# Kernel optimization log

Hardware: AMD Instinct MI355X
Metric: run time of the kernel (lower is better)

The kernel has to match this reference:

```python
import jax, jax.numpy as jnp
import numpy as np

B, S, H, NH = 2, 2048, 1024, 16
HD = H // NH

def setup_inputs() -> dict:
    key = jax.random.key(0)
    ks = jax.random.split(key, 10)
    f = lambda k, shape, scale: jax.random.normal(k, shape, dtype=jnp.float32) * scale
    return {
        "hidden_states": f(ks[0], (B, S, H), 1.0),
        "attention_mask": f(ks[1], (B, 1, S, S), 1.0),
        # static weights: randn * static_ratio(0.9); dynamic: randn * 0.01
        "q_static": f(ks[2], (H, H), 0.9), "q_dynamic": f(ks[3], (H, H), 0.01),
        "k_static": f(ks[4], (H, H), 0.9), "k_dynamic": f(ks[5], (H, H), 0.01),
        "v_static": f(ks[6], (H, H), 0.9), "v_dynamic": f(ks[7], (H, H), 0.01),
        "o_static": f(ks[8], (H, H), 0.9), "o_dynamic": f(ks[9], (H, H), 0.01),
    }

def _split_heads(x):
    # [B, S, H] -> [B, NH, S, HD]
    b, s, _ = x.shape
    return x.reshape(b, s, NH, HD).transpose(0, 2, 1, 3)

def reference(hidden_states, attention_mask,
              q_static, q_dynamic, k_static, k_dynamic,
              v_static, v_dynamic, o_static, o_dynamic):
    # DualWeightLinear: y = x @ (static + dynamic)^T  (no bias)
    q = hidden_states @ (q_static + q_dynamic).T
    k = hidden_states @ (k_static + k_dynamic).T
    v = hidden_states @ (v_static + v_dynamic).T
    q, k, v = _split_heads(q), _split_heads(k), _split_heads(v)  # [B,NH,S,HD]
    scale = 1.0 / np.sqrt(HD).astype(np.float32)
    scores = jnp.einsum('bhqd,bhkd->bhqk', q, k) * scale  # [B,NH,S,S]
    scores = scores + attention_mask  # additive mask, broadcast over heads
    attn = jax.nn.softmax(scores, axis=-1)
    out = jnp.einsum('bhqk,bhkd->bhqd', attn, v)
    out = out.transpose(0, 2, 1, 3).reshape(hidden_states.shape[0], hidden_states.shape[1], H)
    return out @ (o_static + o_dynamic).T
```

## Files before the change

### kernel.cpp

```cpp
#include <hip/hip_runtime.h>
#include <hip/hip_bf16.h>
#include <stdint.h>

#define BB 2
#define SS 2048
#define HH 1024
#define NHH 16
#define HDD 64
#define MM (BB*SS)
#define N4SEG (HH*HH/4)

typedef __attribute__((ext_vector_type(8))) short short8;
typedef __attribute__((ext_vector_type(4))) float f32x4;
typedef __attribute__((ext_vector_type(4))) unsigned short u16x4;
typedef __attribute__((ext_vector_type(4))) unsigned int u32x4;

__device__ __forceinline__ unsigned short f2bf(float x){
  unsigned u = __float_as_uint(x);
  u += 0x7fffu + ((u >> 16) & 1u);
  return (unsigned short)(u >> 16);
}
__device__ __forceinline__ float bf2f(unsigned short h){
  return __uint_as_float(((unsigned)h) << 16);
}
__device__ __forceinline__ unsigned short f2bf_fast(float x){
  __hip_bfloat16 hb = __float2bfloat16(x);
  return *reinterpret_cast<unsigned short*>(&hb);
}

__global__ void k_split(const float* __restrict__ in, unsigned short* __restrict__ hi,
                        unsigned short* __restrict__ lo, int n4){
  int i = blockIdx.x * blockDim.x + threadIdx.x;
  if (i >= n4) return;
  f32x4 x = ((const f32x4*)in)[i];
  u16x4 h, l;
  #pragma unroll
  for (int j = 0; j < 4; ++j){
    unsigned short hb = f2bf(x[j]);
    h[j] = hb;
    l[j] = f2bf(x[j] - bf2f(hb));
  }
  ((u16x4*)hi)[i] = h;
  ((u16x4*)lo)[i] = l;
}

__global__ void k_wprep(const float* __restrict__ qs, const float* __restrict__ qd,
                        const float* __restrict__ ks, const float* __restrict__ kd,
                        const float* __restrict__ vs, const float* __restrict__ vd,
                        const float* __restrict__ os_, const float* __restrict__ od,
                        unsigned short* __restrict__ wqh, unsigned short* __restrict__ wql,
                        unsigned short* __restrict__ wkh, unsigned short* __restrict__ wkl,
                        unsigned short* __restrict__ wv,  unsigned short* __restrict__ wo){
  int i = blockIdx.x * blockDim.x + threadIdx.x;
  int seg = i >> 18;
  int j = i & (N4SEG - 1);
  const float *pa, *pb; unsigned short *ph, *pl = nullptr;
  if      (seg == 0){ pa = qs; pb = qd; ph = wqh; pl = wql; }
  else if (seg == 1){ pa = ks; pb = kd; ph = wkh; pl = wkl; }
  else if (seg == 2){ pa = vs; pb = vd; ph = wv; }
  else              { pa = os_; pb = od; ph = wo; }
  f32x4 x = ((const f32x4*)pa)[j] + ((const f32x4*)pb)[j];
  u16x4 h, l;
  #pragma unroll
  for (int c = 0; c < 4; ++c){
    unsigned short hb = f2bf(x[c]);
    h[c] = hb;
    l[c] = f2bf(x[c] - bf2f(hb));
  }
  ((u16x4*)ph)[j] = h;
  if (pl) ((u16x4*)pl)[j] = l;
}

__global__ __launch_bounds__(256, 2)
void proj_fused(const unsigned short* __restrict__ hsh, const unsigned short* __restrict__ hsl,
                const unsigned short* __restrict__ wqh, const unsigned short* __restrict__ wql,
                const unsigned short* __restrict__ wkh, const unsigned short* __restrict__ wkl,
                const unsigned short* __restrict__ wv,
                unsigned short* __restrict__ qhB, unsigned short* __restrict__ qlB,
                unsigned short* __restrict__ khB, unsigned short* __restrict__ klB,
                unsigned short* __restrict__ vtB)
{
  __shared__ unsigned short Ash[128*32], Asl[128*32], Bsh[128*32], Bsl[128*32];
  const int tid = threadIdx.x;
  const int nb0 = blockIdx.x * 128;
  const int mb0 = blockIdx.y * 128;
  const int kind = nb0 >> 10;
  const int ncol0 = nb0 & 1023;
  const int w  = tid >> 6, lane = tid & 63;
  const int wr = w >> 1,  wc = w & 1;
  const int lg = lane >> 4, lr = lane & 15;

  const unsigned short* Bh = (kind == 0 ? wqh : (kind == 1 ? wkh : wv)) + (size_t)ncol0 * HH;
  const unsigned short* Bl = (kind == 0 ? wql : wkl) + (size_t)ncol0 * HH;
  const unsigned short* Ahb = hsh + (size_t)mb0 * HH;
  const unsigned short* Alb = hsl + (size_t)mb0 * HH;

  f32x4 zero4 = {0.f, 0.f, 0.f, 0.f};
  f32x4 acc[4][4];
  #pragma unroll
  for (int mi = 0; mi < 4; ++mi)
    #pragma unroll
    for (int ni = 0; ni < 4; ++ni) acc[mi][ni] = zero4;

  for (int kb = 0; kb < HH; kb += 32) {
    __syncthreads();
    #pragma unroll
    for (int i = 0; i < 2; ++i){
      int c = i*256 + tid;
      int row = c >> 2, off = (c & 3) << 3;
      size_t go = (size_t)row * HH + kb + off;
      __builtin_amdgcn_global_load_lds(
          (const __attribute__((address_space(1))) void*)(Ahb + go),
          (__attribute__((address_space(3))) void*)(&Ash[c*8]), 16, 0, 0);
      __builtin_amdgcn_global_load_lds(
          (const __attribute__((address_space(1))) void*)(Alb + go),
          (__attribute__((address_space(3))) void*)(&Asl[c*8]), 16, 0, 0);
      __builtin_amdgcn_global_load_lds(
          (const __attribute__((address_space(1))) void*)(Bh + go),
          (__attribute__((address_space(3))) void*)(&Bsh[c*8]), 16, 0, 0);
      if (kind < 2)
        __builtin_amdgcn_global_load_lds(
            (const __attribute__((address_space(1))) void*)(Bl + go),
            (__attribute__((address_space(3))) void*)(&Bsl[c*8]), 16, 0, 0);
    }
    __syncthreads();
    short8 ah4[4], al4[4], bh4[4], bl4[4];
    #pragma unroll
    for (int mi = 0; mi < 4; ++mi){
      int ro = (wr*64 + mi*16 + lr)*32 + lg*8;
      ah4[mi] = *(const short8*)&Ash[ro];
      al4[mi] = *(const short8*)&Asl[ro];
    }
    #pragma unroll
    for (int ni = 0; ni < 4; ++ni){
      int ro = (wc*64 + ni*16 + lr)*32 + lg*8;
      bh4[ni] = *(const short8*)&Bsh[ro];
    }
    if (kind < 2) {
      #pragma unroll
      for (int ni = 0; ni < 4; ++ni){
        int ro = (wc*64 + ni*16 + lr)*32 + lg*8;
        bl4[ni] = *(const short8*)&Bsl[ro];
      }
      #pragma unroll
      for (int mi = 0; mi < 4; ++mi)
        #pragma unroll
        for (int ni = 0; ni < 4; ++ni){
          acc[mi][ni] = __builtin_amdgcn_mfma_f32_16x16x32_bf16(ah4[mi], bh4[ni], acc[mi][ni], 0, 0, 0);
          acc[mi][ni] = __builtin_amdgcn_mfma_f32_16x16x32_bf16(al4[mi], bh4[ni], acc[mi][ni], 0, 0, 0);
          acc[mi][ni] = __builtin_amdgcn_mfma_f32_16x16x32_bf16(ah4[mi], bl4[ni], acc[mi][ni], 0, 0, 0);
        }
    } else {
      #pragma unroll
      for (int mi = 0; mi < 4; ++mi)
        #pragma unroll
        for (int ni = 0; ni < 4; ++ni)
          acc[mi][ni] = __builtin_amdgcn_mfma_f32_16x16x32_bf16(bh4[ni], ah4[mi], acc[mi][ni], 0, 0, 0);
    }
  }

  if (kind == 2) {
    #pragma unroll
    for (int mi = 0; mi < 4; ++mi){
      #pragma unroll
      for (int ni = 0; ni < 4; ++ni){
        int d  = ncol0 + wc*64 + ni*16 + 4*lg;
        int sg = mb0 + wr*64 + mi*16 + lr;
        int b = sg >> 11, s0 = sg & 2047;
        #pragma unroll
        for (int r = 0; r < 4; ++r)
          vtB[((size_t)(b*HH + d + r))*SS + s0] = f2bf_fast(acc[mi][ni][r]);
      }
    }
  } else {
    unsigned short* Ch = (kind == 0) ? qhB : khB;
    unsigned short* Cl = (kind == 0) ? qlB : klB;
    #pragma unroll
    for (int mi = 0; mi < 4; ++mi){
      #pragma unroll
      for (int ni = 0; ni < 4; ++ni){
        int n  = ncol0 + wc*64 + ni*16 + lr;
        int m0 = mb0 + wr*64 + mi*16 + 4*lg;
        #pragma unroll
        for (int r = 0; r < 4; ++r){
          float x = acc[mi][ni][r];
          unsigned short hb = f2bf(x);
          unsigned short lb = f2bf(x - bf2f(hb));
          size_t o = (size_t)(m0 + r)*HH + n;
          Ch[o] = hb;
          Cl[o] = lb;
        }
      }
    }
  }
}

__global__ __launch_bounds__(256, 2)
void gemm_o(const unsigned short* __restrict__ A, const unsigned short* __restrict__ Bm,
            float* __restrict__ C, int M, int N, int K)
{
  __shared__ unsigned short As[128*32];
  __shared__ unsigned short Bs[128*32];
  const int tid = threadIdx.x;
  const int mb0 = blockIdx.y * 128, nb0 = blockIdx.x * 128;
  const int w  = tid >> 6, lane = tid & 63;
  const int wr = w >> 1,  wc = w & 1;
  const int lg = lane >> 4, lr = lane & 15;

  f32x4 zero4 = {0.f, 0.f, 0.f, 0.f};
  f32x4 acc[4][4];
  #pragma unroll
  for (int mi = 0; mi < 4; ++mi)
    #pragma unroll
    for (int ni = 0; ni < 4; ++ni) acc[mi][ni] = zero4;

  const unsigned short* Abase = A  + (size_t)mb0 * K;
  const unsigned short* Bbase = Bm + (size_t)nb0 * K;

  for (int kb = 0; kb < K; kb += 32) {
    __syncthreads();
    #pragma unroll
    for (int i = 0; i < 2; ++i){
      int c = i*256 + tid;
      int row = c >> 2, off = (c & 3) << 3;
      size_t go = (size_t)row * K + kb + off;
      __builtin_amdgcn_global_load_lds(
          (const __attribute__((address_space(1))) void*)(Abase + go),
          (__attribute__((address_space(3))) void*)(&As[c*8]), 16, 0, 0);
      __builtin_amdgcn_global_load_lds(
          (const __attribute__((address_space(1))) void*)(Bbase + go),
          (__attribute__((address_space(3))) void*)(&Bs[c*8]), 16, 0, 0);
    }
    __syncthreads();
    short8 af[4], bfr[4];
    #pragma unroll
    for (int mi = 0; mi < 4; ++mi) af[mi]  = *(const short8*)&As[(wr*64 + mi*16 + lr)*32 + lg*8];
    #pragma unroll
    for (int ni = 0; ni < 4; ++ni) bfr[ni] = *(const short8*)&Bs[(wc*64 + ni*16 + lr)*32 + lg*8];
    #pragma unroll
    for (int mi = 0; mi < 4; ++mi)
      #pragma unroll
      for (int ni = 0; ni < 4; ++ni)
        acc[mi][ni] = __builtin_amdgcn_mfma_f32_16x16x32_bf16(af[mi], bfr[ni], acc[mi][ni], 0, 0, 0);
  }

  #pragma unroll
  for (int mi = 0; mi < 4; ++mi){
    #pragma unroll
    for (int ni = 0; ni < 4; ++ni){
      int n  = nb0 + wc*64 + ni*16 + lr;
      int m0 = mb0 + wr*64 + mi*16 + 4*lg;
      #pragma unroll
      for (int r = 0; r < 4; ++r) C[(size_t)(m0 + r)*N + n] = acc[mi][ni][r];
    }
  }
}

__global__ __launch_bounds__(512, 4)
void attn_fwd(const unsigned short* __restrict__ qh, const unsigned short* __restrict__ ql,
              const unsigned short* __restrict__ kh, const unsigned short* __restrict__ kl,
              const unsigned short* __restrict__ vt, const float* __restrict__ mask,
              unsigned short* __restrict__ ao)
{
  __shared__ unsigned short Ksh[2][64*64];
  __shared__ unsigned short Ksl[2][64*64];
  __shared__ unsigned short Vss[2][64*64];

  const int tid = threadIdx.x;
  const int w = tid >> 6, lane = tid & 63;
  const int lg = lane >> 4, lr = lane & 15;
  const int xork = (lr & 7) << 4;

  const int bid = (blockIdx.x & 7) * 64 + (blockIdx.x >> 3);
  const int qb = bid & 15, h = (bid >> 4) & 15, b = bid >> 8;
  const int q0 = qb*128 + w*16;
  const int hoff = h*64;

  const int srow = tid >> 3;
  const int sgx  = (tid & 7) ^ (srow & 7);

  const int aLO = ((lg & 1)*32 + lr) * 4;
  const int aHI = aLO + 64;
  int addr_c[4];
  #pragma unroll
  for (int r = 0; r < 4; ++r) addr_c[r] = (lg*20 + r) * 4;

  short8 qfh[2], qfl[2];
  {
    size_t qoff = ((size_t)(b*SS + q0 + lr))*HH + hoff + lg*8;
    qfh[0] = *(const short8*)(qh + qoff);
    qfl[0] = *(const short8*)(ql + qoff);
    qfh[1] = *(const short8*)(qh + qoff + 32);
    qfl[1] = *(const short8*)(ql + qoff + 32);
  }
  short8 ones8;
  #pragma unroll
  for (int j = 0; j < 8; ++j) ones8[j] = (short)0x3F80;

  float m_run = -1e30f;
  f32x4 zero4 = {0.f, 0.f, 0.f, 0.f};
  f32x4 acc[4], acc_l = zero4;
  #pragma unroll
  for (int d4 = 0; d4 < 4; ++d4) acc[d4] = zero4;

  const float* mrow = mask + ((size_t)(b*SS + q0 + lr))*SS + 4*lg;

  #define ATTN_STAGE(buf, kvb) do {                                              \
    size_t kro = ((size_t)(b*SS + (kvb) + srow))*HH + hoff + sgx*8;              \
    size_t vro = ((size_t)(b*HH + hoff + srow))*SS + (kvb) + sgx*8;              \
    __builtin_amdgcn_global_load_lds(                                            \
        (const __attribute__((address_space(1))) void*)(kh + kro),               \
        (__attribute__((address_space(3))) void*)(&Ksh[buf][tid*8]), 16, 0, 0);  \
    __builtin_amdgcn_global_load_lds(                                            \
        (const __attribute__((address_space(1))) void*)(kl + kro),               \
        (__attribute__((address_space(3))) void*)(&Ksl[buf][tid*8]), 16, 0, 0);  \
    __builtin_amdgcn_global_load_lds(                                            \
        (const __attribute__((address_space(1))) void*)(vt + vro),               \
        (__attribute__((address_space(3))) void*)(&Vss[buf][tid*8]), 16, 0, 0);  \
  } while (0)

  ATTN_STAGE(0, 0);

  f32x4 mk[4], mk_n[4];
  #pragma unroll
  for (int nb = 0; nb < 4; ++nb) mk[nb] = *(const f32x4*)(mrow + nb*16);

  for (int t = 0; t < SS/64; ++t) {
    const int kv = t*64;
    const int cur = t & 1;
    __syncthreads();
    if (t + 1 < SS/64) {
      ATTN_STAGE(cur ^ 1, kv + 64);
      #pragma unroll
      for (int nb = 0; nb < 4; ++nb) mk_n[nb] = *(const f32x4*)(mrow + kv + 64 + nb*16);
    }

    const int c0 = ((0  + lg*16) ^ xork) >> 1;
    const int c1 = ((64 + lg*16) ^ xork) >> 1;
    f32x4 sc[4];
    __builtin_amdgcn_s_setprio(1);
    #pragma unroll
    for (int nb = 0; nb < 4; ++nb) {
      const int krow = (nb*16 + lr)*64;
      short8 k0h = *(const short8*)&Ksh[cur][krow + c0];
      short8 k1h = *(const short8*)&Ksh[cur][krow + c1];
      short8 k0l = *(const short8*)&Ksl[cur][krow + c0];
      short8 k1l = *(const short8*)&Ksl[cur][krow + c1];
      f32x4 d = zero4;
      d = __builtin_amdgcn_mfma_f32_16x16x32_bf16(k0h, qfh[0], d, 0, 0, 0);
      d = __builtin_amdgcn_mfma_f32_16x16x32_bf16(k1h, qfh[1], d, 0, 0, 0);
      d = __builtin_amdgcn_mfma_f32_16x16x32_bf16(k0l, qfh[0], d, 0, 0, 0);
      d = __builtin_amdgcn_mfma_f32_16x16x32_bf16(k1l, qfh[1], d, 0, 0, 0);
      d = __builtin_amdgcn_mfma_f32_16x16x32_bf16(k0h, qfl[0], d, 0, 0, 0);
      d = __builtin_amdgcn_mfma_f32_16x16x32_bf16(k1h, qfl[1], d, 0, 0, 0);
      sc[nb] = d;
    }
    __builtin_amdgcn_s_setprio(0);

    float s[4][4];
    float rmax = -1e30f;
    #pragma unroll
    for (int nb = 0; nb < 4; ++nb)
      #pragma unroll
      for (int r = 0; r < 4; ++r) {
        float v = fmaf(sc[nb][r], 0.125f, mk[nb][r]);
        s[nb][r] = v;
        rmax = fmaxf(rmax, v);
      }
    rmax = fmaxf(rmax, __shfl_xor(rmax, 16));
    rmax = fmaxf(rmax, __shfl_xor(rmax, 32));

    if (!__all(rmax <= m_run + 8.0f)) {
      float mn = fmaxf(m_run, rmax);
      float corr = __expf(m_run - mn);
      m_run = mn;
      #pragma unroll
      for (int r = 0; r < 4; ++r) {
        float ca = __int_as_float(
            __builtin_amdgcn_ds_bpermute(addr_c[r], __float_as_int(corr)));
        acc_l[r] *= ca;
        #pragma unroll
        for (int d4 = 0; d4 < 4; ++d4) acc[d4][r] *= ca;
      }
    }

    unsigned pw[4][2];
    #pragma unroll
    for (int nb = 0; nb < 4; ++nb) {
      float e0 = __expf(s[nb][0] - m_run);
      float e1 = __expf(s[nb][1] - m_run);
      float e2 = __expf(s[nb][2] - m_run);
      float e3 = __expf(s[nb][3] - m_run);
      pw[nb][0] = (unsigned)f2bf_fast(e0) | ((unsigned)f2bf_fast(e1) << 16);
      pw[nb][1] = (unsigned)f2bf_fast(e2) | ((unsigned)f2bf_fast(e3) << 16);
    }

    const int B0 = lg >> 1;
    u32x4 f0, f1;
    {
      unsigned g0 = __builtin_amdgcn_ds_bpermute(aLO, (int)pw[0][0]);
      unsigned g1 = __builtin_amdgcn_ds_bpermute(aLO, (int)pw[0][1]);
      unsigned g2 = __builtin_amdgcn_ds_bpermute(aLO, (int)pw[1][0]);
      unsigned g3 = __builtin_amdgcn_ds_bpermute(aLO, (int)pw[1][1]);
      unsigned g4 = __builtin_amdgcn_ds_bpermute(aHI, (int)pw[0][0]);
      unsigned g5 = __builtin_amdgcn_ds_bpermute(aHI, (int)pw[0][1]);
      unsigned g6 = __builtin_amdgcn_ds_bpermute(aHI, (int)pw[1][0]);
      unsigned g7 = __builtin_amdgcn_ds_bpermute(aHI, (int)pw[1][1]);
      f0[0] = B0 ? g2 : g0;
      f0[1] = B0 ? g3 : g1;
      f0[2] = B0 ? g6 : g4;
      f0[3] = B0 ? g7 : g5;
    }
    {
      unsigned g0 = __builtin_amdgcn_ds_bpermute(aLO, (int)pw[2][0]);
      unsigned g1 = __builtin_amdgcn_ds_bpermute(aLO, (int)pw[2][1]);
      unsigned g2 = __builtin_amdgcn_ds_bpermute(aLO, (int)pw[3][0]);
      unsigned g3 = __builtin_amdgcn_ds_bpermute(aLO, (int)pw[3][1]);
      unsigned g4 = __builtin_amdgcn_ds_bpermute(aHI, (int)pw[2][0]);
      unsigned g5 = __builtin_amdgcn_ds_bpermute(aHI, (int)pw[2][1]);
      unsigned g6 = __builtin_amdgcn_ds_bpermute(aHI, (int)pw[3][0]);
      unsigned g7 = __builtin_amdgcn_ds_bpermute(aHI, (int)pw[3][1]);
      f1[0] = B0 ? g2 : g0;
      f1[1] = B0 ? g3 : g1;
      f1[2] = B0 ? g6 : g4;
      f1[3] = B0 ? g7 : g5;
    }
    short8 pf0 = *reinterpret_cast<short8*>(&f0);
    short8 pf1 = *reinterpret_cast<short8*>(&f1);

    __builtin_amdgcn_s_setprio(1);
    acc_l = __builtin_amdgcn_mfma_f32_16x16x32_bf16(pf0, ones8, acc_l, 0, 0, 0);
    acc_l = __builtin_amdgcn_mfma_f32_16x16x32_bf16(pf1, ones8, acc_l, 0, 0, 0);
    #pragma unroll
    for (int d4 = 0; d4 < 4; ++d4) {
      const int vrow = (d4*16 + lr)*64;
      short8 vf0 = *(const short8*)&Vss[cur][vrow + c0];
      short8 vf1 = *(const short8*)&Vss[cur][vrow + c1];
      acc[d4] = __builtin_amdgcn_mfma_f32_16x16x32_bf16(pf0, vf0, acc[d4], 0, 0, 0);
      acc[d4] = __builtin_amdgcn_mfma_f32_16x16x32_bf16(pf1, vf1, acc[d4], 0, 0, 0);
    }
    __builtin_amdgcn_s_setprio(0);

    #pragma unroll
    for (int nb = 0; nb < 4; ++nb) mk[nb] = mk_n[nb];
  }
  #undef ATTN_STAGE

  float inv[4];
  #pragma unroll
  for (int r = 0; r < 4; ++r) inv[r] = 1.0f / acc_l[r];
  #pragma unroll
  for (int d4 = 0; d4 < 4; ++d4)
    #pragma unroll
    for (int r = 0; r < 4; ++r) {
      size_t o = ((size_t)(b*SS + q0 + 4*lg + r))*HH + hoff + d4*16 + lr;
      ao[o] = f2bf_fast(acc[d4][r] * inv[r]);
    }
}

extern "C" void kernel_launch(void* const* d_in, const int* in_sizes, int n_in,
                              void* d_out, int out_size, void* d_ws, size_t ws_size,
                              hipStream_t stream)
{
  const float* hs  = (const float*)d_in[0];
  const float* msk = (const float*)d_in[1];
  const float* qs  = (const float*)d_in[2];
  const float* qd  = (const float*)d_in[3];
  const float* ks  = (const float*)d_in[4];
  const float* kd  = (const float*)d_in[5];
  const float* vs  = (const float*)d_in[6];
  const float* vd  = (const float*)d_in[7];
  const float* os_ = (const float*)d_in[8];
  const float* od  = (const float*)d_in[9];
  float* out = (float*)d_out;

  const size_t NHS = (size_t)MM * HH;
  const size_t NW  = (size_t)HH * HH;
  unsigned short* p = (unsigned short*)d_ws;
  unsigned short* hsh = p; p += NHS;
  unsigned short* hsl = p; p += NHS;
  unsigned short* wqh = p; p += NW;
  unsigned short* wql = p; p += NW;
  unsigned short* wkh = p; p += NW;
  unsigned short* wkl = p; p += NW;
  unsigned short* wv  = p; p += NW;
  unsigned short* wo  = p; p += NW;
  unsigned short* qhB = p; p += NHS;
  unsigned short* qlB = p; p += NHS;
  unsigned short* khB = p; p += NHS;
  unsigned short* klB = p; p += NHS;
  unsigned short* vtB = p; p += NHS;
  unsigned short* aoB = p; p += NHS;

  k_split<<<(int)(NHS/1024), 256, 0, stream>>>(hs, hsh, hsl, (int)(NHS/4));
  k_wprep<<<(int)(4*N4SEG/256), 256, 0, stream>>>(qs, qd, ks, kd, vs, vd, os_, od,
                                                  wqh, wql, wkh, wkl, wv, wo);

  proj_fused<<<dim3(3*HH/128, MM/128), 256, 0, stream>>>(hsh, hsl, wqh, wql, wkh, wkl, wv,
                                                         qhB, qlB, khB, klB, vtB);

  attn_fwd<<<BB*NHH*(SS/128), 512, 0, stream>>>(qhB, qlB, khB, klB, vtB, msk, aoB);

  gemm_o<<<dim3(HH/128, MM/128), 256, 0, stream>>>(aoB, wo, out, MM, HH, HH);
}
```

Measured before the change: 336.9 us.

## Halve attention block size and load V fragments directly from global memory

The attention kernel now runs 256-thread blocks covering 64 queries instead of 512 threads covering 128, which doubles the grid. V is no longer staged in LDS; each wave loads its V fragments straight from global memory into registers on every kv step. K high/low tiles are still staged in LDS with two loads per thread. This cuts LDS use and barrier cost, but V is re-read from global/L2 by every wave, and the direct loads are issued in the same iteration they are consumed, so their latency may be exposed.

```diff
diff --git a/kernel.cpp b/kernel.cpp
--- a/kernel.cpp
+++ b/kernel.cpp
@@ -256,7 +256,7 @@
   }
 }
 
-__global__ __launch_bounds__(512, 4)
+__global__ __launch_bounds__(256, 4)
 void attn_fwd(const unsigned short* __restrict__ qh, const unsigned short* __restrict__ ql,
               const unsigned short* __restrict__ kh, const unsigned short* __restrict__ kl,
               const unsigned short* __restrict__ vt, const float* __restrict__ mask,
@@ -264,20 +264,19 @@
 {
   __shared__ unsigned short Ksh[2][64*64];
   __shared__ unsigned short Ksl[2][64*64];
-  __shared__ unsigned short Vss[2][64*64];
 
   const int tid = threadIdx.x;
   const int w = tid >> 6, lane = tid & 63;
   const int lg = lane >> 4, lr = lane & 15;
   const int xork = (lr & 7) << 4;
 
-  const int bid = (blockIdx.x & 7) * 64 + (blockIdx.x >> 3);
-  const int qb = bid & 15, h = (bid >> 4) & 15, b = bid >> 8;
-  const int q0 = qb*128 + w*16;
+  const int bid = (blockIdx.x & 7) * 128 + (blockIdx.x >> 3);
+  const int qb = bid & 31, h = (bid >> 5) & 15, b = bid >> 9;
+  const int q0 = qb*64 + w*16;
   const int hoff = h*64;
 
-  const int srow = tid >> 3;
-  const int sgx  = (tid & 7) ^ (srow & 7);
+  const int srow0 = tid >> 3;
+  const int sgx   = (tid & 7) ^ (srow0 & 7);
 
   const int aLO = ((lg & 1)*32 + lr) * 4;
   const int aHI = aLO + 64;
@@ -297,6 +296,11 @@
   #pragma unroll
   for (int j = 0; j < 8; ++j) ones8[j] = (short)0x3F80;
 
+  const unsigned short* vp[4];
+  #pragma unroll
+  for (int d4 = 0; d4 < 4; ++d4)
+    vp[d4] = vt + ((size_t)(b*HH + hoff + d4*16 + lr))*SS + 8*lg;
+
   float m_run = -1e30f;
   f32x4 zero4 = {0.f, 0.f, 0.f, 0.f};
   f32x4 acc[4], acc_l = zero4;
@@ -305,18 +309,21 @@
 
   const float* mrow = mask + ((size_t)(b*SS + q0 + lr))*SS + 4*lg;
 
-  #define ATTN_STAGE(buf, kvb) do {                                              \
-    size_t kro = ((size_t)(b*SS + (kvb) + srow))*HH + hoff + sgx*8;              \
-    size_t vro = ((size_t)(b*HH + hoff + srow))*SS + (kvb) + sgx*8;              \
-    __builtin_amdgcn_global_load_lds(                                            \
-        (const __attribute__((address_space(1))) void*)(kh + kro),               \
-        (__attribute__((address_space(3))) void*)(&Ksh[buf][tid*8]), 16, 0, 0);  \
-    __builtin_amdgcn_global_load_lds(                                            \
-        (const __attribute__((address_space(1))) void*)(kl + kro),               \
-        (__attribute__((address_space(3))) void*)(&Ksl[buf][tid*8]), 16, 0, 0);  \
-    __builtin_amdgcn_global_load_lds(                                            \
-        (const __attribute__((address_space(1))) void*)(vt + vro),               \
-        (__attribute__((address_space(3))) void*)(&Vss[buf][tid*8]), 16, 0, 0);  \
+  #define ATTN_STAGE(buf, kvb) do {                                                  \
+    size_t kro0 = ((size_t)(b*SS + (kvb) + srow0))*HH + hoff + sgx*8;                \
+    size_t kro1 = ((size_t)(b*SS + (kvb) + 32 + srow0))*HH + hoff + sgx*8;           \
+    __builtin_amdgcn_global_load_lds(                                                \
+        (const __attribute__((address_space(1))) void*)(kh + kro0),                  \
+        (__attribute__((address_space(3))) void*)(&Ksh[buf][tid*8]), 16, 0, 0);      \
+    __builtin_amdgcn_global_load_lds(                                                \
+        (const __attribute__((address_space(1))) void*)(kh + kro1),                  \
+        (__attribute__((address_space(3))) void*)(&Ksh[buf][2048 + tid*8]), 16, 0, 0); \
+    __builtin_amdgcn_global_load_lds(                                                \
+        (const __attribute__((address_space(1))) void*)(kl + kro0),                  \
+        (__attribute__((address_space(3))) void*)(&Ksl[buf][tid*8]), 16, 0, 0);      \
+    __builtin_amdgcn_global_load_lds(                                                \
+        (const __attribute__((address_space(1))) void*)(kl + kro1),                  \
+        (__attribute__((address_space(3))) void*)(&Ksl[buf][2048 + tid*8]), 16, 0, 0); \
   } while (0)
 
   ATTN_STAGE(0, 0);
@@ -333,6 +340,13 @@
       ATTN_STAGE(cur ^ 1, kv + 64);
       #pragma unroll
       for (int nb = 0; nb < 4; ++nb) mk_n[nb] = *(const f32x4*)(mrow + kv + 64 + nb*16);
+    }
+
+    short8 vg0[4], vg1[4];
+    #pragma unroll
+    for (int d4 = 0; d4 < 4; ++d4) {
+      vg0[d4] = *(const short8*)(vp[d4] + kv);
+      vg1[d4] = *(const short8*)(vp[d4] + kv + 32);
     }
 
     const int c0 = ((0  + lg*16) ^ xork) >> 1;
@@ -433,11 +447,8 @@
     acc_l = __builtin_amdgcn_mfma_f32_16x16x32_bf16(pf1, ones8, acc_l, 0, 0, 0);
     #pragma unroll
     for (int d4 = 0; d4 < 4; ++d4) {
-      const int vrow = (d4*16 + lr)*64;
-      short8 vf0 = *(const short8*)&Vss[cur][vrow + c0];
-      short8 vf1 = *(const short8*)&Vss[cur][vrow + c1];
-      acc[d4] = __builtin_amdgcn_mfma_f32_16x16x32_bf16(pf0, vf0, acc[d4], 0, 0, 0);
-      acc[d4] = __builtin_amdgcn_mfma_f32_16x16x32_bf16(pf1, vf1, acc[d4], 0, 0, 0);
+      acc[d4] = __builtin_amdgcn_mfma_f32_16x16x32_bf16(pf0, vg0[d4], acc[d4], 0, 0, 0);
+      acc[d4] = __builtin_amdgcn_mfma_f32_16x16x32_bf16(pf1, vg1[d4], acc[d4], 0, 0, 0);
     }
     __builtin_amdgcn_s_setprio(0);
 
@@ -499,7 +510,7 @@
   proj_fused<<<dim3(3*HH/128, MM/128), 256, 0, stream>>>(hsh, hsl, wqh, wql, wkh, wkl, wv,
                                                          qhB, qlB, khB, klB, vtB);
 
-  attn_fwd<<<BB*NHH*(SS/128), 512, 0, stream>>>(qhB, qlB, khB, klB, vtB, msk, aoB);
+  attn_fwd<<<BB*NHH*(SS/64), 256, 0, stream>>>(qhB, qlB, khB, klB, vtB, msk, aoB);
 
   gemm_o<<<dim3(HH/128, MM/128), 256, 0, stream>>>(aoB, wo, out, MM, HH, HH);
 }
```

New measurement: 470.1 us. 39.5% more time.
